# Performance work log

Measured on AMD Instinct MI355X. Metric: run time of the kernel, lower is better.

The kernel has to match this reference:

```python
import jax, jax.numpy as jnp
from jax import lax
import numpy as np

H = 512  # hidden size
D = 2    # per-step input/output size


def _lstm_cell(x, h, c, Wih, Whh, b):
    # torch LSTMCell gate order: i, f, g, o
    gates = x @ Wih.T + h @ Whh.T + b  # [B, 4H]
    i, f, g, o = jnp.split(gates, 4, axis=-1)
    i = jax.nn.sigmoid(i)
    f = jax.nn.sigmoid(f)
    g = jnp.tanh(g)
    o = jax.nn.sigmoid(o)
    c_new = f * c + i * g
    h_new = o * jnp.tanh(c_new)
    return h_new, c_new


def setup_inputs() -> dict:
    key = jax.random.key(0)
    ks = jax.random.split(key, 12)
    B, T = 1024, 64
    s = 1.0 / np.sqrt(H)  # torch LSTMCell init scale
    inp = {
        "x": jax.random.normal(ks[0], (B, 2 * T), dtype=jnp.float32),
        "Wih1": jax.random.uniform(ks[1], (4 * H, D), jnp.float32, -s, s),
        "Whh1": jax.random.uniform(ks[2], (4 * H, H), jnp.float32, -s, s),
        "b1": jax.random.uniform(ks[3], (4 * H,), jnp.float32, -s, s),
        "Wih2": jax.random.uniform(ks[4], (4 * H, H), jnp.float32, -s, s),
        "Whh2": jax.random.uniform(ks[5], (4 * H, H), jnp.float32, -s, s),
        "b2": jax.random.uniform(ks[6], (4 * H,), jnp.float32, -s, s),
        "Wl": jax.random.uniform(ks[7], (D, H), jnp.float32, -s, s),
        "bl": jax.random.uniform(ks[8], (D,), jnp.float32, -s, s),
        "future": 32,
    }
    return inp


def reference(x, Wih1, Whh1, b1, Wih2, Whh2, b2, Wl, bl, future):
    B = x.shape[0]
    T = x.shape[1] // 2
    xs = x.reshape(B, T, D).swapaxes(0, 1)  # [T, B, 2] time-major

    z = jnp.zeros((B, H), dtype=x.dtype)
    init = (z, z, z, z)

    def obs_step(carry, xt):
        h1, c1, h2, c2 = carry
        h1, c1 = _lstm_cell(xt, h1, c1, Wih1, Whh1, b1)
        h2, c2 = _lstm_cell(h1, h2, c2, Wih2, Whh2, b2)
        out = h2 @ Wl.T + bl  # [B, 2]
        return (h1, c1, h2, c2), out

    carry, outs = lax.scan(obs_step, init, xs)  # outs: [T, B, 2]

    if future > 1:
        def fut_step(carry, _):
            h1, c1, h2, c2, out = carry
            h1, c1 = _lstm_cell(out, h1, c1, Wih1, Whh1, b1)
            h2, c2 = _lstm_cell(h1, h2, c2, Wih2, Whh2, b2)
            out = h2 @ Wl.T + bl
            return (h1, c1, h2, c2, out), out

        _, fouts = lax.scan(fut_step, (*carry, outs[-1]), None, length=future - 1)
        outs = jnp.concatenate([outs, fouts], axis=0)  # [T+future-1, B, 2]

    # torch.cat(outputs, dim=1) -> [B, 2*(T+future-1)]
    return outs.swapaxes(0, 1).reshape(B, -1)
```

## Files before the change

### kernel.cpp

```cpp
#include <hip/hip_runtime.h>
#include <cstdint>
#include <cstddef>

typedef unsigned short u16;
typedef int i32x4 __attribute__((ext_vector_type(4)));

static constexpr int HID    = 512;
static constexpr int BATCH  = 1024;
static constexpr int NSTEPS = 95;
static constexpr int T_OBS  = 64;
static constexpr int OUTW   = 190;

#define SQRT512 22.627416997969522
#define WQ ((float)(32512.0 * SQRT512))
static constexpr float HQ = 32512.f;
#define GSC ((float)(1.0 / (SQRT512 * 32512.0 * 32512.0)))

__device__ __forceinline__ float sigm(float x) { return 1.f / (1.f + __expf(-x)); }
__device__ __forceinline__ float tanh_fast(float x) {
  float ax = fabsf(x);
  float t  = __expf(-2.f * ax);
  float r  = (1.f - t) / (1.f + t);
  return x < 0.f ? -r : r;
}

typedef __attribute__((address_space(1))) const uint32_t glb_u32;
typedef __attribute__((address_space(3))) uint32_t lds_u32;
__device__ __forceinline__ void glds16(const void* g, void* l) {
  __builtin_amdgcn_global_load_lds((glb_u32*)g, (lds_u32*)l, 16, 0, 0);
}

__global__ void prep_btx1(const float* __restrict__ Whh1, char* __restrict__ Bt) {
  int idx = blockIdx.x * 256 + threadIdx.x;
  int n = idx >> 10, t = idx & 1023;
  int blk = t >> 7, rem = t & 127;
  int s = rem >> 4, e = rem & 15;
  int c = s ^ (n & 7);
  int k = blk * 64 + (c & 3) * 16 + e;
  int r = (n & 3) * HID + (n >> 2);
  int w = (int)rintf(Whh1[r * HID + k] * WQ);
  int hi = (w + 128) >> 8, lo = w - (hi << 8);
  Bt[idx] = (char)((c < 4) ? hi : lo);
}
__global__ void prep_btx2(const float* __restrict__ Wih2, const float* __restrict__ Whh2,
                          char* __restrict__ Bt) {
  int idx = blockIdx.x * 256 + threadIdx.x;
  int n = idx >> 11, t = idx & 2047;
  int blk = t >> 7, rem = t & 127;
  int s = rem >> 4, e = rem & 15;
  int c = s ^ (n & 7);
  int k = blk * 64 + (c & 3) * 16 + e;
  int r = (n & 3) * HID + (n >> 2);
  float v = (k < 512) ? Wih2[r * HID + k] : Whh2[r * HID + (k - 512)];
  int w = (int)rintf(v * WQ);
  int hi = (w + 128) >> 8, lo = w - (hi << 8);
  Bt[idx] = (char)((c < 4) ? hi : lo);
}
__global__ void prep_small(const float* __restrict__ b1, const float* __restrict__ b2,
                           const float* __restrict__ Wih1,
                           float* __restrict__ b1p, float* __restrict__ b2p,
                           float* __restrict__ w1p) {
  int n = blockIdx.x * 256 + threadIdx.x;
  if (n >= 2048) return;
  int r = (n & 3) * HID + (n >> 2);
  b1p[n] = b1[r];
  b2p[n] = b2[r];
  w1p[2 * n + 0] = Wih1[2 * r + 0];
  w1p[2 * n + 1] = Wih1[2 * r + 1];
}
__global__ void init_out(const float* __restrict__ bl, float* __restrict__ out) {
  int i = blockIdx.x * 256 + threadIdx.x;
  if (i < BATCH * OUTW) out[i] = bl[i & 1];
}

struct GArgs {
  const char* Ax0; const char* Ax1;
  const char* Bt;
  const float* bias;
  const float* xptr; int xstride;
  const float* wih;
  char* Hx;
  float* CstT;
  const float* wl;
  float* oacc;
};

#define MFMA8_(A, B, C) C = __builtin_amdgcn_mfma_i32_16x16x64_i8(A, B, C, 0, 0, 0)

#define STAGE(KS, SLOT)                                                         \
  {                                                                             \
    char* const AsU_ = smem + (SLOT) * 16384;                                   \
    char* const BsU_ = smem + (SLOT) * 16384 + 8192;                            \
    const char* ap_ = (KTOT == 1024 && (KS) >= 8) ? aR2 : aR;                   \
    const int ablk_ = (KTOT == 1024) ? ((KS) & 7) : (KS);                       \
    _Pragma("unroll")                                                           \
    for (int i_ = 0; i_ < 2; ++i_) {                                            \
      const int gi_ = wid * 2 + i_;                  \
      glds16(ap_ + (size_t)(8 * gi_) * 1024 + ablk_ * 128, AsU_ + gi_ * 1024);  \
      glds16(bR + (size_t)(8 * gi_) * BRS + (size_t)(KS) * 128, BsU_ + gi_ * 1024);\
    }                                                                           \
  }

#define KKBODY(SLOT)                                                            \
  {                                                                             \
    const char* const Ab_ = smem + (SLOT) * 16384;                              \
    const char* const Bb_ = Ab_ + 8192;                                         \
    const i32x4 ah0_ = *(const i32x4*)(Ab_ + (wm * 32 +  0 + l15) * 128 + so0);          \
    const i32x4 ah1_ = *(const i32x4*)(Ab_ + (wm * 32 + 16 + l15) * 128 + so0);          \
    const i32x4 bh0_ = *(const i32x4*)(Bb_ + (wn * 32 +  0 + l15) * 128 + so0);          \
    const i32x4 bh1_ = *(const i32x4*)(Bb_ + (wn * 32 + 16 + l15) * 128 + so0);          \
    MFMA8_(bh0_, ah0_, p00); MFMA8_(bh0_, ah1_, p01);                           \
    MFMA8_(bh1_, ah0_, p10); MFMA8_(bh1_, ah1_, p11);                           \
    const i32x4 bl0_ = *(const i32x4*)(Bb_ + (wn * 32 +  0 + l15) * 128 + (so0 ^ 64));   \
    const i32x4 bl1_ = *(const i32x4*)(Bb_ + (wn * 32 + 16 + l15) * 128 + (so0 ^ 64));   \
    MFMA8_(bl0_, ah0_, q00); MFMA8_(bl0_, ah1_, q01);                           \
    MFMA8_(bl1_, ah0_, q10); MFMA8_(bl1_, ah1_, q11);                           \
    const i32x4 al0_ = *(const i32x4*)(Ab_ + (wm * 32 +  0 + l15) * 128 + (so0 ^ 64));   \
    const i32x4 al1_ = *(const i32x4*)(Ab_ + (wm * 32 + 16 + l15) * 128 + (so0 ^ 64));   \
    MFMA8_(bh0_, al0_, q00); MFMA8_(bh0_, al1_, q01);                           \
    MFMA8_(bh1_, al0_, q10); MFMA8_(bh1_, al1_, q11);                           \
    MFMA8_(bl0_, al0_, r00); MFMA8_(bl0_, al1_, r01);                           \
    MFMA8_(bl1_, al0_, r10); MFMA8_(bl1_, al1_, r11);                           \
  }

#define EPI(I, J, P, Q, R)                                                      \
  {                                                                             \
    const int hl_ = wn * 8 + (I) * 4 + lq;                                      \
    const int hg_ = hg0 + hl_;                                                  \
    const int ml_ = wm * 32 + (J) * 16 + l15;                                   \
    const int mg_ = mg0 + ml_;                                                  \
    const float4 b4_ = *(const float4*)(bias + 4 * hg_);                        \
    float g0_ = ((float)P[0] * 65536.f + (float)Q[0] * 256.f + (float)R[0]) * GSC + b4_.x; \
    float g1_ = ((float)P[1] * 65536.f + (float)Q[1] * 256.f + (float)R[1]) * GSC + b4_.y; \
    float g2_ = ((float)P[2] * 65536.f + (float)Q[2] * 256.f + (float)R[2]) * GSC + b4_.z; \
    float g3_ = ((float)P[3] * 65536.f + (float)Q[3] * 256.f + (float)R[3]) * GSC + b4_.w; \
    if (HASX) {                                                                 \
      const float x0_ = xptr[(size_t)mg_ * xstride + 0];                        \
      const float x1_ = xptr[(size_t)mg_ * xstride + 1];                        \
      const float4 wA_ = *(const float4*)(wih + 8 * hg_);                       \
      const float4 wB_ = *(const float4*)(wih + 8 * hg_ + 4);                   \
      g0_ += x0_ * wA_.x + x1_ * wA_.y;  g1_ += x0_ * wA_.z + x1_ * wA_.w;      \
      g2_ += x0_ * wB_.x + x1_ * wB_.y;  g3_ += x0_ * wB_.z + x1_ * wB_.w;      \
    }                                                                           \
    const float ig_ = sigm(g0_), fg_ = sigm(g1_);                               \
    const float gg_ = tanh_fast(g2_), og_ = sigm(g3_);                          \
    float* cp_ = CstT + (size_t)hg_ * BATCH + mg_;                              \
    const float cn_ = fg_ * (*cp_) + ig_ * gg_;                                 \
    *cp_ = cn_;                                                                 \
    const float hn_ = og_ * tanh_fast(cn_);                                     \
    Hsh[ml_ * 17 + hl_] = (u16)(short)(int)rintf(hn_ * HQ);                     \
    if (PROJ) {                                                                 \
      if ((J) == 0) { s0a += hn_ * wl[hg_]; s1a += hn_ * wl[HID + hg_]; }       \
      else          { s0b += hn_ * wl[hg_]; s1b += hn_ * wl[HID + hg_]; }       \
    }                                                                           \
  }

template <int KTOT, bool HASX, bool PROJ>
__device__ __forceinline__ void run_gemm(const GArgs& g, int mt, int nt, char* smem) {
  const char* const Ax0 = g.Ax0;  const char* const Ax1 = g.Ax1;
  const char* const Bt  = g.Bt;
  const float* const bias = g.bias;
  const float* const xptr = g.xptr; const int xstride = g.xstride;
  const float* const wih  = g.wih;
  float* const CstT = g.CstT;
  char* const Hx = g.Hx;
  const float* const wl = g.wl;
  float* const oacc = g.oacc;

  const int tid = threadIdx.x;
  const int wid = tid >> 6, lane = tid & 63;
  const int wm = wid >> 1, wn = wid & 1;
  const int l15 = lane & 15, lq = lane >> 4;
  const int so0 = ((lq ^ (l15 & 7)) & 7) << 4;
  const int lrow8 = lane >> 3;
  const int lslot8 = lane & 7;

  const char* const aR = Ax0 + (size_t)(mt * 64 + lrow8) * 1024 + lslot8 * 16;
  const char* const aR2 = (KTOT == 1024)
      ? (Ax1 + (size_t)(mt * 64 + lrow8) * 1024 + lslot8 * 16) : aR;
  constexpr int BRS = 2 * KTOT;
  const char* const bR = Bt + (size_t)(nt * 64 + lrow8) * BRS + lslot8 * 16;

  i32x4 p00 = {}, p01 = {}, p10 = {}, p11 = {};
  i32x4 q00 = {}, q01 = {}, q10 = {}, q11 = {};
  i32x4 r00 = {}, r01 = {}, r10 = {}, r11 = {};
  constexpr int TOT = KTOT / 64;

  STAGE(0, 0);
  STAGE(1, 1);
  STAGE(2, 2);
  for (int ks = 0; ks < TOT; ++ks) {
    if (ks < TOT - 2) {
      asm volatile("s_waitcnt vmcnt(8)" ::: "memory");
    } else if (ks < TOT - 1) {
      asm volatile("s_waitcnt vmcnt(4)" ::: "memory");
    } else {
      asm volatile("s_waitcnt vmcnt(0)" ::: "memory");
    }
    __builtin_amdgcn_s_barrier();
    if (ks + 3 < TOT) STAGE(ks + 3, (ks + 3) & 3);
    KKBODY(ks & 3);
  }

  __syncthreads();
  u16* const Hsh = (u16*)smem;

  const int mg0 = mt * 64, hg0 = nt * 16;
  float s0a = 0.f, s1a = 0.f, s0b = 0.f, s1b = 0.f;

  EPI(0, 0, p00, q00, r00); EPI(1, 0, p10, q10, r10);
  EPI(0, 1, p01, q01, r01); EPI(1, 1, p11, q11, r11);

  if (PROJ) {
    s0a += __shfl_xor(s0a, 16); s0a += __shfl_xor(s0a, 32);
    s1a += __shfl_xor(s1a, 16); s1a += __shfl_xor(s1a, 32);
    s0b += __shfl_xor(s0b, 16); s0b += __shfl_xor(s0b, 32);
    s1b += __shfl_xor(s1b, 16); s1b += __shfl_xor(s1b, 32);
    if (lq == 0) {
      int mgA = mg0 + wm * 32 + l15;
      unsafeAtomicAdd(&oacc[(size_t)mgA * OUTW + 0], s0a);
      unsafeAtomicAdd(&oacc[(size_t)mgA * OUTW + 1], s1a);
      int mgB = mgA + 16;
      unsafeAtomicAdd(&oacc[(size_t)mgB * OUTW + 0], s0b);
      unsafeAtomicAdd(&oacc[(size_t)mgB * OUTW + 1], s1b);
    }
  }

  __syncthreads();
#pragma unroll
  for (int q = 0; q < 2; ++q) {
    const int m = (tid >> 3) + 32 * q;
    const int pr = tid & 7;
    const int hg = hg0 + pr * 2;
    const int mg = mg0 + m;
    const int v0 = (int)(short)Hsh[m * 17 + pr * 2];
    const int v1 = (int)(short)Hsh[m * 17 + pr * 2 + 1];
    const int h0 = (v0 + 128) >> 8, l0 = v0 - (h0 << 8);
    const int h1 = (v1 + 128) >> 8, l1 = v1 - (h1 << 8);
    const int blk = hg >> 6, kk = hg & 63;
    const int c = kk >> 4, e = kk & 15;
    const int sh = c ^ (mg & 7);
    char* rowp = Hx + (size_t)mg * 1024 + blk * 128;
    *(u16*)(rowp + sh * 16 + e)       = (u16)((h0 & 255) | ((h1 & 255) << 8));
    *(u16*)(rowp + (sh ^ 4) * 16 + e) = (u16)((l0 & 255) | ((l1 & 255) << 8));
  }
}

#define TILE_MAP(b)                                                            \
  const int g8_ = (b) & 7, j_ = (b) >> 3;                                      \
  const int nt = (g8_ & 3) * 8 + (j_ & 7);                                     \
  const int mt = (g8_ >> 2) * 8 + (j_ >> 3);

template <int KTOT, bool HASX, bool PROJ>
__global__ __launch_bounds__(256, 2) void step_single(GArgs ga) {
  __shared__ __align__(16) char smem[65536];
  TILE_MAP(blockIdx.x);
  run_gemm<KTOT, HASX, PROJ>(ga, mt, nt, smem);
}

__global__ __launch_bounds__(256, 2) void step_fused(GArgs g2, GArgs g1) {
  __shared__ __align__(16) char smem[65536];
  const int bid = blockIdx.x;
  const int g8_ = bid & 7;
  const int grp = bid >> 3;
  const int role = grp & 1;
  const int j_ = grp >> 1;
  const int nt = (g8_ & 3) * 8 + (j_ & 7);
  const int mt = (g8_ >> 2) * 8 + (j_ >> 3);
  if (role == 0) run_gemm<1024, false, true>(g2, mt, nt, smem);
  else           run_gemm<512, true, false>(g1, mt, nt, smem);
}

extern "C" void kernel_launch(void* const* d_in, const int* in_sizes, int n_in,
                              void* d_out, int out_size, void* d_ws, size_t ws_size,
                              hipStream_t stream) {
  const float* x    = (const float*)d_in[0];
  const float* Wih1 = (const float*)d_in[1];
  const float* Whh1 = (const float*)d_in[2];
  const float* b1   = (const float*)d_in[3];
  const float* Wih2 = (const float*)d_in[4];
  const float* Whh2 = (const float*)d_in[5];
  const float* b2   = (const float*)d_in[6];
  const float* Wl   = (const float*)d_in[7];
  const float* bl   = (const float*)d_in[8];
  float* out = (float*)d_out;
  (void)in_sizes; (void)n_in; (void)out_size; (void)ws_size;

  char* p = (char*)d_ws;
  auto alloc = [&](size_t bytes) -> char* {
    char* r = p; p += (bytes + 255) & ~(size_t)255; return r;
  };
  char* Bt1 = alloc((size_t)2048 * 1024);
  char* Bt2 = alloc((size_t)2048 * 2048);
  char* state0 = p;
  char* Hxb[4];
  for (int i = 0; i < 4; ++i) Hxb[i] = alloc((size_t)BATCH * 1024);
  float* C1 = (float*)alloc((size_t)BATCH * HID * 4);
  float* C2 = (float*)alloc((size_t)BATCH * HID * 4);
  size_t state_bytes = (size_t)(p - state0);
  float* b1p = (float*)alloc(2048 * 4);
  float* b2p = (float*)alloc(2048 * 4);
  float* w1p = (float*)alloc(2048 * 2 * 4);

  hipMemsetAsync(state0, 0, state_bytes, stream);
  init_out<<<(BATCH * OUTW + 255) / 256, 256, 0, stream>>>(bl, out);
  prep_btx1<<<8192, 256, 0, stream>>>(Whh1, Bt1);
  prep_btx2<<<16384, 256, 0, stream>>>(Wih2, Whh2, Bt2);
  prep_small<<<8, 256, 0, stream>>>(b1, b2, Wih1, b1p, b2p, w1p);

  auto mkL1 = [&](int t) -> GArgs {
    int par = t & 1, prev = par ^ 1;
    GArgs a{};
    a.Ax0 = Hxb[0 + prev]; a.Ax1 = nullptr;
    a.Bt = Bt1; a.bias = b1p;
    a.xptr = (t < T_OBS) ? (x + 2 * t) : (out + 2 * (t - 1));
    a.xstride = (t < T_OBS) ? (2 * T_OBS) : OUTW;
    a.wih = w1p; a.CstT = C1;
    a.Hx = Hxb[0 + par];
    a.wl = nullptr; a.oacc = nullptr;
    return a;
  };
  auto mkL2 = [&](int t) -> GArgs {
    int par = t & 1, prev = par ^ 1;
    GArgs a{};
    a.Ax0 = Hxb[0 + par];
    a.Ax1 = Hxb[2 + prev];
    a.Bt = Bt2; a.bias = b2p;
    a.xptr = nullptr; a.xstride = 0; a.wih = nullptr;
    a.CstT = C2;
    a.Hx = Hxb[2 + par];
    a.wl = Wl; a.oacc = out + 2 * t;
    return a;
  };

  step_single<512, true, false><<<512, 256, 0, stream>>>(mkL1(0));
  for (int t = 0; t < T_OBS - 1; ++t)
    step_fused<<<1024, 256, 0, stream>>>(mkL2(t), mkL1(t + 1));
  step_single<1024, false, true><<<512, 256, 0, stream>>>(mkL2(T_OBS - 1));
  for (int t = T_OBS; t < NSTEPS; ++t) {
    step_single<512, true, false><<<512, 256, 0, stream>>>(mkL1(t));
    step_single<1024, false, true><<<512, 256, 0, stream>>>(mkL2(t));
  }
}
```

Baseline: 2.687 ms.

## Replace LDS-direct async loads with register-staged double buffering, raise occupancy

Replaces the global_load_lds direct-to-LDS 4-slot pipeline with a register-staged scheme. Two register sets hold the next K-slices while the current slice is written to one of three LDS slots, with a barrier before each MFMA body. LDS per block drops from 64KB to 48KB and launch bounds rise to 3 blocks per CU, aiming for more concurrent blocks to hide latency. The cost is extra VGPR pressure, LDS write instructions, and shallower prefetch depth.

Measured after the change: 2.718 ms. About the same (+1.1%).

```diff
diff --git a/kernel.cpp b/kernel.cpp
--- a/kernel.cpp
+++ b/kernel.cpp
@@ -22,12 +22,6 @@
   float t  = __expf(-2.f * ax);
   float r  = (1.f - t) / (1.f + t);
   return x < 0.f ? -r : r;
-}
-
-typedef __attribute__((address_space(1))) const uint32_t glb_u32;
-typedef __attribute__((address_space(3))) uint32_t lds_u32;
-__device__ __forceinline__ void glds16(const void* g, void* l) {
-  __builtin_amdgcn_global_load_lds((glb_u32*)g, (lds_u32*)l, 16, 0, 0);
 }
 
 __global__ void prep_btx1(const float* __restrict__ Whh1, char* __restrict__ Bt) {
@@ -87,18 +81,29 @@
 
 #define MFMA8_(A, B, C) C = __builtin_amdgcn_mfma_i32_16x16x64_i8(A, B, C, 0, 0, 0)
 
-#define STAGE(KS, SLOT)                                                         \
+#define STAGE_LOAD(R, KS)                                                       \
+  {                                                                             \
+    const char* ap_ = (KTOT == 1024 && (KS) >= 8) ? aR2 : aR;                   \
+    const int ablk_ = (KTOT == 1024) ? ((KS) & 7) : (KS);                       \
+    R##a0 = *(const uint4*)(ap_ + (size_t)(8 * (wid * 2 + 0)) * 1024 + ablk_ * 128);   \
+    R##a1 = *(const uint4*)(ap_ + (size_t)(8 * (wid * 2 + 1)) * 1024 + ablk_ * 128);   \
+    R##b0 = *(const uint4*)(bR + (size_t)(8 * (wid * 2 + 0)) * BRS + (size_t)(KS) * 128); \
+    R##b1 = *(const uint4*)(bR + (size_t)(8 * (wid * 2 + 1)) * BRS + (size_t)(KS) * 128); \
+  }
+#define STAGE_WRITE(R, SLOT)                                                    \
   {                                                                             \
     char* const AsU_ = smem + (SLOT) * 16384;                                   \
     char* const BsU_ = smem + (SLOT) * 16384 + 8192;                            \
-    const char* ap_ = (KTOT == 1024 && (KS) >= 8) ? aR2 : aR;                   \
-    const int ablk_ = (KTOT == 1024) ? ((KS) & 7) : (KS);                       \
-    _Pragma("unroll")                                                           \
-    for (int i_ = 0; i_ < 2; ++i_) {                                            \
-      const int gi_ = wid * 2 + i_;                  \
-      glds16(ap_ + (size_t)(8 * gi_) * 1024 + ablk_ * 128, AsU_ + gi_ * 1024);  \
-      glds16(bR + (size_t)(8 * gi_) * BRS + (size_t)(KS) * 128, BsU_ + gi_ * 1024);\
-    }                                                                           \
+    *(uint4*)(AsU_ + (wid * 2 + 0) * 1024 + lane * 16) = R##a0;                 \
+    *(uint4*)(AsU_ + (wid * 2 + 1) * 1024 + lane * 16) = R##a1;                 \
+    *(uint4*)(BsU_ + (wid * 2 + 0) * 1024 + lane * 16) = R##b0;                 \
+    *(uint4*)(BsU_ + (wid * 2 + 1) * 1024 + lane * 16) = R##b1;                 \
+  }
+#define RBAR()                                                                  \
+  {                                                                             \
+    asm volatile("s_waitcnt lgkmcnt(0)" ::: "memory");                          \
+    __builtin_amdgcn_s_barrier();                                               \
+    __builtin_amdgcn_sched_barrier(0);                                          \
   }
 
 #define KKBODY(SLOT)                                                            \
@@ -186,20 +191,22 @@
   i32x4 r00 = {}, r01 = {}, r10 = {}, r11 = {};
   constexpr int TOT = KTOT / 64;
 
-  STAGE(0, 0);
-  STAGE(1, 1);
-  STAGE(2, 2);
-  for (int ks = 0; ks < TOT; ++ks) {
-    if (ks < TOT - 2) {
-      asm volatile("s_waitcnt vmcnt(8)" ::: "memory");
-    } else if (ks < TOT - 1) {
-      asm volatile("s_waitcnt vmcnt(4)" ::: "memory");
-    } else {
-      asm volatile("s_waitcnt vmcnt(0)" ::: "memory");
-    }
-    __builtin_amdgcn_s_barrier();
-    if (ks + 3 < TOT) STAGE(ks + 3, (ks + 3) & 3);
-    KKBODY(ks & 3);
+  uint4 sAa0, sAa1, sAb0, sAb1;
+  uint4 sBa0, sBa1, sBb0, sBb1;
+  STAGE_LOAD(sA, 0);
+  STAGE_LOAD(sB, 1);
+  int slA = 0, slB = 1;
+  for (int kk = 0; kk < TOT; kk += 2) {
+    STAGE_WRITE(sA, slA);
+    if (kk + 2 < TOT) STAGE_LOAD(sA, kk + 2);
+    RBAR();
+    KKBODY(slA);
+    STAGE_WRITE(sB, slB);
+    if (kk + 3 < TOT) STAGE_LOAD(sB, kk + 3);
+    RBAR();
+    KKBODY(slB);
+    slA += 2; if (slA >= 3) slA -= 3;
+    slB += 2; if (slB >= 3) slB -= 3;
   }
 
   __syncthreads();
@@ -237,8 +244,8 @@
     const int v1 = (int)(short)Hsh[m * 17 + pr * 2 + 1];
     const int h0 = (v0 + 128) >> 8, l0 = v0 - (h0 << 8);
     const int h1 = (v1 + 128) >> 8, l1 = v1 - (h1 << 8);
-    const int blk = hg >> 6, kk = hg & 63;
-    const int c = kk >> 4, e = kk & 15;
+    const int blk = hg >> 6, kq = hg & 63;
+    const int c = kq >> 4, e = kq & 15;
     const int sh = c ^ (mg & 7);
     char* rowp = Hx + (size_t)mg * 1024 + blk * 128;
     *(u16*)(rowp + sh * 16 + e)       = (u16)((h0 & 255) | ((h1 & 255) << 8));
@@ -252,14 +259,14 @@
   const int mt = (g8_ >> 2) * 8 + (j_ >> 3);
 
 template <int KTOT, bool HASX, bool PROJ>
-__global__ __launch_bounds__(256, 2) void step_single(GArgs ga) {
-  __shared__ __align__(16) char smem[65536];
+__global__ __launch_bounds__(256, 3) void step_single(GArgs ga) {
+  __shared__ __align__(16) char smem[49152];
   TILE_MAP(blockIdx.x);
   run_gemm<KTOT, HASX, PROJ>(ga, mt, nt, smem);
 }
 
-__global__ __launch_bounds__(256, 2) void step_fused(GArgs g2, GArgs g1) {
-  __shared__ __align__(16) char smem[65536];
+__global__ __launch_bounds__(256, 3) void step_fused(GArgs g2, GArgs g1) {
+  __shared__ __align__(16) char smem[49152];
   const int bid = blockIdx.x;
   const int g8_ = bid & 7;
   const int grp = bid >> 3;
```

## Drop low×low int8 product term and restage K loop as 128-wide double buffer

Applied to the files above, without the earlier changes.

Removes the r accumulators (the low-byte × low-byte MFMA partial products) from the split-int8 GEMM, cutting a quarter of the MFMAs and dropping their contribution from the gate sum. The K loop is also restaged to load 128-wide K slices into two 32KB buffers with a plain double buffer, replacing the 4-slot, 3-deep prefetch pipeline that used explicit vmcnt waits. The dropped term slightly reduces numerical precision of the gate pre-activations. The shallower prefetch may expose more global-load latency.

New measurement: 2.645 ms. About the same (-1.6%).

```diff
diff --git a/kernel.cpp b/kernel.cpp
--- a/kernel.cpp
+++ b/kernel.cpp
@@ -89,51 +89,49 @@
 
 #define STAGE(KS, SLOT)                                                         \
   {                                                                             \
-    char* const AsU_ = smem + (SLOT) * 16384;                                   \
-    char* const BsU_ = smem + (SLOT) * 16384 + 8192;                            \
-    const char* ap_ = (KTOT == 1024 && (KS) >= 8) ? aR2 : aR;                   \
-    const int ablk_ = (KTOT == 1024) ? ((KS) & 7) : (KS);                       \
+    char* const AsU_ = smem + (SLOT) * 32768;                                   \
+    char* const BsU_ = smem + (SLOT) * 32768 + 16384;                           \
+    const char* ap_ = (KTOT == 1024 && (KS) >= 4) ? aR2 : aR;                   \
+    const int ablk_ = (KTOT == 1024) ? ((KS) & 3) : (KS);                       \
     _Pragma("unroll")                                                           \
-    for (int i_ = 0; i_ < 2; ++i_) {                                            \
-      const int gi_ = wid * 2 + i_;                  \
-      glds16(ap_ + (size_t)(8 * gi_) * 1024 + ablk_ * 128, AsU_ + gi_ * 1024);  \
-      glds16(bR + (size_t)(8 * gi_) * BRS + (size_t)(KS) * 128, BsU_ + gi_ * 1024);\
+    for (int i_ = 0; i_ < 4; ++i_) {                                            \
+      const int gi_ = wid * 4 + i_;                 \
+      glds16(ap_ + (size_t)(4 * gi_) * 1024 + ablk_ * 256, AsU_ + gi_ * 1024);  \
+      glds16(bR + (size_t)(4 * gi_) * BRS + (size_t)(KS) * 256, BsU_ + gi_ * 1024);\
     }                                                                           \
   }
 
-#define KKBODY(SLOT)                                                            \
+#define KKBODY(SLOT, HF)                                                        \
   {                                                                             \
-    const char* const Ab_ = smem + (SLOT) * 16384;                              \
-    const char* const Bb_ = Ab_ + 8192;                                         \
-    const i32x4 ah0_ = *(const i32x4*)(Ab_ + (wm * 32 +  0 + l15) * 128 + so0);          \
-    const i32x4 ah1_ = *(const i32x4*)(Ab_ + (wm * 32 + 16 + l15) * 128 + so0);          \
-    const i32x4 bh0_ = *(const i32x4*)(Bb_ + (wn * 32 +  0 + l15) * 128 + so0);          \
-    const i32x4 bh1_ = *(const i32x4*)(Bb_ + (wn * 32 + 16 + l15) * 128 + so0);          \
+    const char* const Ab_ = smem + (SLOT) * 32768 + (HF) * 128;                 \
+    const char* const Bb_ = smem + (SLOT) * 32768 + 16384 + (HF) * 128;        \
+    const i32x4 ah0_ = *(const i32x4*)(Ab_ + (wm * 32 +  0 + l15) * 256 + so0);          \
+    const i32x4 ah1_ = *(const i32x4*)(Ab_ + (wm * 32 + 16 + l15) * 256 + so0);          \
+    const i32x4 bh0_ = *(const i32x4*)(Bb_ + (wn * 32 +  0 + l15) * 256 + so0);          \
+    const i32x4 bh1_ = *(const i32x4*)(Bb_ + (wn * 32 + 16 + l15) * 256 + so0);          \
     MFMA8_(bh0_, ah0_, p00); MFMA8_(bh0_, ah1_, p01);                           \
     MFMA8_(bh1_, ah0_, p10); MFMA8_(bh1_, ah1_, p11);                           \
-    const i32x4 bl0_ = *(const i32x4*)(Bb_ + (wn * 32 +  0 + l15) * 128 + (so0 ^ 64));   \
-    const i32x4 bl1_ = *(const i32x4*)(Bb_ + (wn * 32 + 16 + l15) * 128 + (so0 ^ 64));   \
+    const i32x4 bl0_ = *(const i32x4*)(Bb_ + (wn * 32 +  0 + l15) * 256 + (so0 ^ 64));   \
+    const i32x4 bl1_ = *(const i32x4*)(Bb_ + (wn * 32 + 16 + l15) * 256 + (so0 ^ 64));   \
     MFMA8_(bl0_, ah0_, q00); MFMA8_(bl0_, ah1_, q01);                           \
     MFMA8_(bl1_, ah0_, q10); MFMA8_(bl1_, ah1_, q11);                           \
-    const i32x4 al0_ = *(const i32x4*)(Ab_ + (wm * 32 +  0 + l15) * 128 + (so0 ^ 64));   \
-    const i32x4 al1_ = *(const i32x4*)(Ab_ + (wm * 32 + 16 + l15) * 128 + (so0 ^ 64));   \
+    const i32x4 al0_ = *(const i32x4*)(Ab_ + (wm * 32 +  0 + l15) * 256 + (so0 ^ 64));   \
+    const i32x4 al1_ = *(const i32x4*)(Ab_ + (wm * 32 + 16 + l15) * 256 + (so0 ^ 64));   \
     MFMA8_(bh0_, al0_, q00); MFMA8_(bh0_, al1_, q01);                           \
     MFMA8_(bh1_, al0_, q10); MFMA8_(bh1_, al1_, q11);                           \
-    MFMA8_(bl0_, al0_, r00); MFMA8_(bl0_, al1_, r01);                           \
-    MFMA8_(bl1_, al0_, r10); MFMA8_(bl1_, al1_, r11);                           \
-  }
-
-#define EPI(I, J, P, Q, R)                                                      \
+  }
+
+#define EPI(I, J, P, Q)                                                         \
   {                                                                             \
     const int hl_ = wn * 8 + (I) * 4 + lq;                                      \
     const int hg_ = hg0 + hl_;                                                  \
     const int ml_ = wm * 32 + (J) * 16 + l15;                                   \
     const int mg_ = mg0 + ml_;                                                  \
     const float4 b4_ = *(const float4*)(bias + 4 * hg_);                        \
-    float g0_ = ((float)P[0] * 65536.f + (float)Q[0] * 256.f + (float)R[0]) * GSC + b4_.x; \
-    float g1_ = ((float)P[1] * 65536.f + (float)Q[1] * 256.f + (float)R[1]) * GSC + b4_.y; \
-    float g2_ = ((float)P[2] * 65536.f + (float)Q[2] * 256.f + (float)R[2]) * GSC + b4_.z; \
-    float g3_ = ((float)P[3] * 65536.f + (float)Q[3] * 256.f + (float)R[3]) * GSC + b4_.w; \
+    float g0_ = ((float)P[0] * 65536.f + (float)Q[0] * 256.f) * GSC + b4_.x;    \
+    float g1_ = ((float)P[1] * 65536.f + (float)Q[1] * 256.f) * GSC + b4_.y;    \
+    float g2_ = ((float)P[2] * 65536.f + (float)Q[2] * 256.f) * GSC + b4_.z;    \
+    float g3_ = ((float)P[3] * 65536.f + (float)Q[3] * 256.f) * GSC + b4_.w;    \
     if (HASX) {                                                                 \
       const float x0_ = xptr[(size_t)mg_ * xstride + 0];                        \
       const float x1_ = xptr[(size_t)mg_ * xstride + 1];                        \
@@ -172,34 +170,25 @@
   const int wm = wid >> 1, wn = wid & 1;
   const int l15 = lane & 15, lq = lane >> 4;
   const int so0 = ((lq ^ (l15 & 7)) & 7) << 4;
-  const int lrow8 = lane >> 3;
-  const int lslot8 = lane & 7;
-
-  const char* const aR = Ax0 + (size_t)(mt * 64 + lrow8) * 1024 + lslot8 * 16;
+  const int lrow4 = lane >> 4;
+  const int lslot16 = lane & 15;
+
+  const char* const aR = Ax0 + (size_t)(mt * 64 + lrow4) * 1024 + lslot16 * 16;
   const char* const aR2 = (KTOT == 1024)
-      ? (Ax1 + (size_t)(mt * 64 + lrow8) * 1024 + lslot8 * 16) : aR;
+      ? (Ax1 + (size_t)(mt * 64 + lrow4) * 1024 + lslot16 * 16) : aR;
   constexpr int BRS = 2 * KTOT;
-  const char* const bR = Bt + (size_t)(nt * 64 + lrow8) * BRS + lslot8 * 16;
+  const char* const bR = Bt + (size_t)(nt * 64 + lrow4) * BRS + lslot16 * 16;
 
   i32x4 p00 = {}, p01 = {}, p10 = {}, p11 = {};
   i32x4 q00 = {}, q01 = {}, q10 = {}, q11 = {};
-  i32x4 r00 = {}, r01 = {}, r10 = {}, r11 = {};
-  constexpr int TOT = KTOT / 64;
+  constexpr int TOT = KTOT / 128;
 
   STAGE(0, 0);
-  STAGE(1, 1);
-  STAGE(2, 2);
   for (int ks = 0; ks < TOT; ++ks) {
-    if (ks < TOT - 2) {
-      asm volatile("s_waitcnt vmcnt(8)" ::: "memory");
-    } else if (ks < TOT - 1) {
-      asm volatile("s_waitcnt vmcnt(4)" ::: "memory");
-    } else {
-      asm volatile("s_waitcnt vmcnt(0)" ::: "memory");
-    }
-    __builtin_amdgcn_s_barrier();
-    if (ks + 3 < TOT) STAGE(ks + 3, (ks + 3) & 3);
-    KKBODY(ks & 3);
+    __syncthreads();
+    if (ks + 1 < TOT) STAGE(ks + 1, (ks + 1) & 1);
+    KKBODY(ks & 1, 0);
+    KKBODY(ks & 1, 1);
   }
 
   __syncthreads();
@@ -208,8 +197,8 @@
   const int mg0 = mt * 64, hg0 = nt * 16;
   float s0a = 0.f, s1a = 0.f, s0b = 0.f, s1b = 0.f;
 
-  EPI(0, 0, p00, q00, r00); EPI(1, 0, p10, q10, r10);
-  EPI(0, 1, p01, q01, r01); EPI(1, 1, p11, q11, r11);
+  EPI(0, 0, p00, q00); EPI(1, 0, p10, q10);
+  EPI(0, 1, p01, q01); EPI(1, 1, p11, q11);
 
   if (PROJ) {
     s0a += __shfl_xor(s0a, 16); s0a += __shfl_xor(s0a, 32);
@@ -237,8 +226,8 @@
     const int v1 = (int)(short)Hsh[m * 17 + pr * 2 + 1];
     const int h0 = (v0 + 128) >> 8, l0 = v0 - (h0 << 8);
     const int h1 = (v1 + 128) >> 8, l1 = v1 - (h1 << 8);
-    const int blk = hg >> 6, kk = hg & 63;
-    const int c = kk >> 4, e = kk & 15;
+    const int blk = hg >> 6, kq = hg & 63;
+    const int c = kq >> 4, e = kq & 15;
     const int sh = c ^ (mg & 7);
     char* rowp = Hx + (size_t)mg * 1024 + blk * 128;
     *(u16*)(rowp + sh * 16 + e)       = (u16)((h0 & 255) | ((h1 & 255) << 8));
```
